# Kernel optimization log

Measured on AMD Instinct MI355X. Metric: run time of the kernel, lower is better.

Reference implementation:

```python
import jax, jax.numpy as jnp
import numpy as np

N = 100000
IN_DIM = 128
HID = 32
HEADS = 2
DEG = 16
NEG_SLOPE = 0.2


def setup_inputs() -> dict:
    rng = np.random.default_rng(0)
    E_rand = N * DEG
    src = np.concatenate([rng.integers(0, N, E_rand), np.arange(N)]).astype(np.int64)
    dst = np.concatenate([rng.integers(0, N, E_rand), np.arange(N)]).astype(np.int64)

    key = jax.random.key(0)
    ks = jax.random.split(key, 10)
    feat = jax.random.normal(ks[0], (N, IN_DIM), dtype=jnp.float32)
    # layer 1: in_dim -> HEADS * HID
    W1 = jax.random.normal(ks[1], (IN_DIM, HEADS * HID), dtype=jnp.float32) / np.sqrt(IN_DIM)
    al1 = jax.random.normal(ks[2], (HEADS, HID), dtype=jnp.float32) * 0.1
    ar1 = jax.random.normal(ks[3], (HEADS, HID), dtype=jnp.float32) * 0.1
    b1 = jnp.zeros((HEADS * HID,), dtype=jnp.float32)
    # layer 2: HEADS*HID -> 1 * HID
    W2 = jax.random.normal(ks[4], (HEADS * HID, HID), dtype=jnp.float32) / np.sqrt(HEADS * HID)
    al2 = jax.random.normal(ks[5], (1, HID), dtype=jnp.float32) * 0.1
    ar2 = jax.random.normal(ks[6], (1, HID), dtype=jnp.float32) * 0.1
    b2 = jnp.zeros((HID,), dtype=jnp.float32)
    return {"feat": feat, "W1": W1, "al1": al1, "ar1": ar1, "b1": b1,
            "W2": W2, "al2": al2, "ar2": ar2, "b2": b2,
            "src": jnp.asarray(src), "dst": jnp.asarray(dst)}


def gat_conv(feat, W, al, ar, b, src, dst, n_nodes, activation=True):
    # DGL GATConv: fc (no bias) -> per-head dot with attn vecs -> leaky_relu
    # edge score -> softmax over incoming edges of each dst -> scatter-add -> +bias -> relu
    H, D = al.shape
    h = (feat @ W).reshape(-1, H, D)                       # [N,H,D]
    el = jnp.einsum('nhd,hd->nh', h, al)                   # [N,H]
    er = jnp.einsum('nhd,hd->nh', h, ar)                   # [N,H]
    e = jax.nn.leaky_relu(el[src] + er[dst], NEG_SLOPE)    # [E,H]
    m = jax.ops.segment_max(e, dst, num_segments=n_nodes)  # [N,H]
    e = jnp.exp(e - jax.lax.stop_gradient(m)[dst])
    s = jax.ops.segment_sum(e, dst, num_segments=n_nodes)  # [N,H]
    a = e / s[dst]                                         # [E,H]
    msg = h[src] * a[:, :, None]                           # [E,H,D]
    out = jax.ops.segment_sum(msg, dst, num_segments=n_nodes)  # [N,H,D]
    out = out + b.reshape(1, H, D)
    return jax.nn.relu(out) if activation else out


def reference(feat, W1, al1, ar1, b1, W2, al2, ar2, b2, src, dst):
    h = gat_conv(feat, W1, al1, ar1, b1, src, dst, N)      # [N,HEADS,HID]
    h = h.reshape(h.shape[0], -1)                          # [N,HEADS*HID]
    h = gat_conv(h, W2, al2, ar2, b2, src, dst, N)         # [N,1,HID]
    return h.squeeze(1)                                    # [N,HID]
```

## Files before the change

### kernel.cpp

```cpp
#include <hip/hip_runtime.h>
#include <hip/hip_fp16.h>
#include <math.h>


constexpr int CAP  = 64;
constexpr int MAXB = 512;
constexpr int TILE = 2048;
constexpr int BCAP = 5120;

typedef _Float16 f16x8 __attribute__((ext_vector_type(8)));
typedef float    f32x4 __attribute__((ext_vector_type(4)));

__global__ __launch_bounds__(256)
void k_prew(const float* __restrict__ W1, const float* __restrict__ al1, const float* __restrict__ ar1,
            const float* __restrict__ W2, const float* __restrict__ al2, const float* __restrict__ ar2,
            _Float16* __restrict__ vh1, _Float16* __restrict__ B2h, int* __restrict__ gcur)
{
    const int t = threadIdx.x;
    for (int i = t; i < 128 * 16; i += 256) {
        const int k = i >> 4, c = i & 15;
        float s = 0.f;
        if (c < 4) {
            const int h = c & 1;
            const float* a = (c >> 1) ? ar1 : al1;
            #pragma unroll
            for (int d = 0; d < 32; d++) s += W1[k * 64 + h * 32 + d] * a[h * 32 + d];
        }
        vh1[i] = (_Float16)s;
    }
    for (int i = t; i < 64 * 64; i += 256) {
        const int k = i >> 6, c = i & 63;
        float s = 0.f;
        if (c < 32) s = W2[k * 32 + c];
        else if (c < 34) {
            const float* a = (c == 32) ? al2 : ar2;
            #pragma unroll
            for (int d = 0; d < 32; d++) s += W2[k * 32 + d] * a[d];
        }
        B2h[i] = (_Float16)s;
    }
    for (int b = t; b < MAXB; b += 256) gcur[b] = 0;
}

__global__ __launch_bounds__(256)
void k_front(const int* __restrict__ src, const int* __restrict__ dst,
             int* __restrict__ gcur, unsigned* __restrict__ binbuf, int E, int Gbin,
             const float* __restrict__ x, const float* __restrict__ W,
             const _Float16* __restrict__ vh1,
             __half* __restrict__ h1, float* __restrict__ el, float* __restrict__ er,
             int nnodes)
{
    __shared__ alignas(16) char smem[32 * 1024];
    const int tid = threadIdx.x;

    if ((int)blockIdx.x < Gbin) {
        int* cnt  = (int*)smem;
        int* base = cnt + MAXB;
        for (int b = tid; b < MAXB; b += 256) cnt[b] = 0;
        __syncthreads();
        const int e0 = blockIdx.x * TILE;
        int lo[8]; unsigned rec[8]; int bn[8];
        #pragma unroll
        for (int u = 0; u < 8; u++) {
            const int e = e0 + u * 256 + tid;
            if (e < E) {
                const int d = dst[e];
                bn[u]  = d >> 8;
                rec[u] = ((unsigned)src[e] << 8) | (unsigned)(d & 255);
                lo[u]  = atomicAdd(&cnt[bn[u]], 1);
            } else bn[u] = -1;
        }
        __syncthreads();
        for (int b = tid; b < MAXB; b += 256) {
            const int c = cnt[b];
            base[b] = c ? atomicAdd(&gcur[b], c) : 0;
        }
        __syncthreads();
        #pragma unroll
        for (int u = 0; u < 8; u++) if (bn[u] >= 0) {
            const int p = base[bn[u]] + lo[u];
            if ((unsigned)p < (unsigned)BCAP)
                binbuf[(long)bn[u] * BCAP + p] = rec[u];
        }
        return;
    }

    _Float16* xs = (_Float16*)smem;
    _Float16* Wh = xs + 64 * 128;
    const int node0 = ((int)blockIdx.x - Gbin) * 64;

    for (int c = tid; c < 1024; c += 256) {
        const int row = c >> 4, k8 = c & 15;
        const int n = node0 + row;
        float4 v0 = make_float4(0, 0, 0, 0), v1 = v0;
        if (n < nnodes) {
            v0 = ((const float4*)x)[(long)n * 32 + k8 * 2];
            v1 = ((const float4*)x)[(long)n * 32 + k8 * 2 + 1];
        }
        f16x8 h;
        h[0] = v0.x; h[1] = v0.y; h[2] = v0.z; h[3] = v0.w;
        h[4] = v1.x; h[5] = v1.y; h[6] = v1.z; h[7] = v1.w;
        const int off = (row * 256 + k8 * 16) ^ ((row & 7) << 4);
        *(f16x8*)((char*)xs + off) = h;
    }
    for (int c = tid; c < 1024; c += 256) {
        const int k = c >> 3, j8 = (c & 7) * 8;
        float4 v0 = ((const float4*)W)[(k * 64 + j8) >> 2];
        float4 v1 = ((const float4*)W)[((k * 64 + j8) >> 2) + 1];
        f16x8 h;
        h[0] = v0.x; h[1] = v0.y; h[2] = v0.z; h[3] = v0.w;
        h[4] = v1.x; h[5] = v1.y; h[6] = v1.z; h[7] = v1.w;
        *(f16x8*)(Wh + k * 64 + j8) = h;
    }
    __syncthreads();

    const int wv = tid >> 6, l = tid & 63;
    const int col = wv * 16 + (l & 15);
    const int g = l >> 4;
    f16x8 bfr[4], vfr[4];
    #pragma unroll
    for (int t = 0; t < 4; t++)
        #pragma unroll
        for (int e = 0; e < 8; e++)
            bfr[t][e] = Wh[(t * 32 + g * 8 + e) * 64 + col];
    if (wv == 0) {
        #pragma unroll
        for (int t = 0; t < 4; t++)
            #pragma unroll
            for (int e = 0; e < 8; e++)
                vfr[t][e] = vh1[(t * 32 + g * 8 + e) * 16 + (l & 15)];
    }

    #pragma unroll
    for (int nt = 0; nt < 4; nt++) {
        f32x4 acc = {0.f, 0.f, 0.f, 0.f}, accv = {0.f, 0.f, 0.f, 0.f};
        const int row = nt * 16 + (l & 15);
        #pragma unroll
        for (int t = 0; t < 4; t++) {
            const int off = (row * 256 + (t * 32 + g * 8) * 2) ^ ((row & 7) << 4);
            f16x8 af = *(const f16x8*)((const char*)xs + off);
            acc = __builtin_amdgcn_mfma_f32_16x16x32_f16(af, bfr[t], acc, 0, 0, 0);
            if (wv == 0)
                accv = __builtin_amdgcn_mfma_f32_16x16x32_f16(af, vfr[t], accv, 0, 0, 0);
        }
        #pragma unroll
        for (int r = 0; r < 4; r++) {
            const int n = node0 + nt * 16 + g * 4 + r;
            if (n < nnodes) {
                h1[(long)n * 64 + col] = __float2half((float)acc[r]);
                if (wv == 0) {
                    const int c4 = l & 15;
                    if (c4 < 2)      el[n * 2 + c4]       = (float)accv[r];
                    else if (c4 < 4) er[n * 2 + (c4 - 2)] = (float)accv[r];
                }
            }
        }
    }
}

__global__ __launch_bounds__(256)
void k_scatter(const unsigned* __restrict__ binbuf, const int* __restrict__ gcur,
               int* __restrict__ deg, int* __restrict__ bucket, int nnodes)
{
    extern __shared__ int lds[];
    int* ldeg  = lds;
    int* lbuck = lds + 256;
    const int t = threadIdx.x, b = blockIdx.x;
    const int nb0 = b << 8;
    ldeg[t] = 0;
    __syncthreads();
    const int cnt = min(max(gcur[b], 0), BCAP);
    const unsigned* recs = binbuf + (long)b * BCAP;
    for (int i = t; i < cnt; i += 256) {
        const unsigned r = recs[i];
        const int nl  = (int)(r & 255u);
        const int pos = atomicAdd(&ldeg[nl], 1);
        if (pos < CAP) lbuck[nl * CAP + pos] = (int)(r >> 8);
    }
    __syncthreads();
    const int nv = min(256, nnodes - nb0);
    if (t < nv) deg[nb0 + t] = ldeg[t];
    const int tot4 = nv * (CAP / 4);
    int4* gb = (int4*)(bucket + (long)nb0 * CAP);
    const int4* lb = (const int4*)lbuck;
    for (int i = t; i < tot4; i += 256) gb[i] = lb[i];
}

__global__ __launch_bounds__(256)
void k_agg1(const __half* __restrict__ hbuf, const float* __restrict__ el,
            const float* __restrict__ er, const int* __restrict__ deg,
            const int* __restrict__ bucket, const float* __restrict__ b1,
            __half* __restrict__ o1, int nnodes)
{
    constexpr int OUT = 64;
    const int w = threadIdx.x >> 6, lane = threadIdx.x & 63;
    const int n = blockIdx.x * 4 + w;
    __shared__ int    sbuf[4][CAP];
    __shared__ float2 wbuf[4][CAP];
    if (n >= nnodes) return;

    const int dn = min(deg[n], CAP);
    const int sv = (lane < dn) ? bucket[(long)n * CAP + lane] : 0;
    sbuf[w][lane] = sv;

    const float2 ernv = ((const float2*)er)[n];
    const float2 elv  = ((const float2*)el)[sv];
    float e0 = elv.x + ernv.x; e0 = (e0 > 0.f) ? e0 : 0.2f * e0;
    float e1 = elv.y + ernv.y; e1 = (e1 > 0.f) ? e1 : 0.2f * e1;
    const float w0 = (lane < dn) ? __expf(e0) : 0.f;
    const float w1 = (lane < dn) ? __expf(e1) : 0.f;
    wbuf[w][lane] = make_float2(w0, w1);
    float s0 = w0, s1 = w1;
    #pragma unroll
    for (int off = 32; off; off >>= 1) {
        s0 += __shfl_xor(s0, off, 64);
        s1 += __shfl_xor(s1, off, 64);
    }
    const float inv0 = (s0 > 0.f) ? 1.f / s0 : 0.f;
    const float inv1 = (s1 > 0.f) ? 1.f / s1 : 0.f;

    const int q = lane >> 3, c8 = lane & 7, hh = c8 >> 2;
    const float invC = hh ? inv1 : inv0;
    float acc[8] = {0.f,0.f,0.f,0.f,0.f,0.f,0.f,0.f};
    for (int i = 0; i < dn; i += 16) {
        const int   sA = sbuf[w][i + q],                     sB = sbuf[w][i + 8 + q];
        const float wA = ((const float*)&wbuf[w][i + q])[hh];
        const float wB = ((const float*)&wbuf[w][i + 8 + q])[hh];
        union { float4 f4; __half2 h2v[4]; } uA, uB;
        uA.f4 = *(const float4*)(hbuf + (long)sA * OUT + c8 * 8);
        uB.f4 = *(const float4*)(hbuf + (long)sB * OUT + c8 * 8);
        #pragma unroll
        for (int j = 0; j < 4; j++) {
            const float2 xa = __half22float2(uA.h2v[j]);
            const float2 xb = __half22float2(uB.h2v[j]);
            acc[2*j]   = fmaf(xa.x, wA, acc[2*j]);
            acc[2*j+1] = fmaf(xa.y, wA, acc[2*j+1]);
            acc[2*j]   = fmaf(xb.x, wB, acc[2*j]);
            acc[2*j+1] = fmaf(xb.y, wB, acc[2*j+1]);
        }
    }
    #pragma unroll
    for (int j = 0; j < 8; j++) {
        acc[j] += __shfl_xor(acc[j], 8, 64);
        acc[j] += __shfl_xor(acc[j], 16, 64);
        acc[j] += __shfl_xor(acc[j], 32, 64);
    }
    if (q == 0) {
        f16x8 ov;
        #pragma unroll
        for (int j = 0; j < 8; j++)
            ov[j] = (_Float16)fmaxf(acc[j] * invC + b1[c8 * 8 + j], 0.f);
        *(f16x8*)((char*)o1 + (long)n * 128 + c8 * 16) = ov;
    }
}

__global__ __launch_bounds__(256)
void k_gemm2(const __half* __restrict__ o1, const _Float16* __restrict__ B2h,
             __half* __restrict__ h2, float* __restrict__ el2, float* __restrict__ er2,
             int nnodes)
{
    __shared__ _Float16 xs[64 * 64];
    const int tid = threadIdx.x;
    const int node0 = blockIdx.x * 64;

    for (int c = tid; c < 512; c += 256) {
        const int row = c >> 3, k8 = c & 7;
        const int n = node0 + row;
        f16x8 h = {0,0,0,0,0,0,0,0};
        if (n < nnodes) h = *(const f16x8*)((const char*)o1 + (long)n * 128 + k8 * 16);
        const int off = (row * 128 + k8 * 16) ^ ((row & 7) << 4);
        *(f16x8*)((char*)xs + off) = h;
    }
    __syncthreads();

    const int wv = tid >> 6, l = tid & 63;
    if (wv == 3) return;
    const int col = wv * 16 + (l & 15);
    const int g = l >> 4;
    f16x8 bfr[2];
    #pragma unroll
    for (int t = 0; t < 2; t++)
        #pragma unroll
        for (int e = 0; e < 8; e++)
            bfr[t][e] = B2h[(t * 32 + g * 8 + e) * 64 + col];

    #pragma unroll
    for (int nt = 0; nt < 4; nt++) {
        f32x4 acc = {0.f, 0.f, 0.f, 0.f};
        const int row = nt * 16 + (l & 15);
        #pragma unroll
        for (int t = 0; t < 2; t++) {
            const int off = (row * 128 + (t * 32 + g * 8) * 2) ^ ((row & 7) << 4);
            f16x8 af = *(const f16x8*)((const char*)xs + off);
            acc = __builtin_amdgcn_mfma_f32_16x16x32_f16(af, bfr[t], acc, 0, 0, 0);
        }
        #pragma unroll
        for (int r = 0; r < 4; r++) {
            const int n = node0 + nt * 16 + g * 4 + r;
            if (n < nnodes) {
                if (wv < 2) h2[(long)n * 32 + col] = __float2half((float)acc[r]);
                else {
                    const int c4 = l & 15;
                    if (c4 == 0)      el2[n] = (float)acc[r];
                    else if (c4 == 1) er2[n] = (float)acc[r];
                }
            }
        }
    }
}

__global__ __launch_bounds__(256)
void k_agg2(const __half* __restrict__ h2, const float* __restrict__ el2,
            const float* __restrict__ er2, const int* __restrict__ deg,
            const int* __restrict__ bucket, const float* __restrict__ b2,
            float* __restrict__ out, int nnodes)
{
    const int w = threadIdx.x >> 6, lane = threadIdx.x & 63;
    const int n = blockIdx.x * 4 + w;
    __shared__ int   sbuf[4][CAP];
    __shared__ float wbuf[4][CAP];
    if (n >= nnodes) return;

    const int dn = min(deg[n], CAP);
    const int sv = (lane < dn) ? bucket[(long)n * CAP + lane] : 0;
    sbuf[w][lane] = sv;

    const float ern = er2[n];
    float e = el2[sv] + ern; e = (e > 0.f) ? e : 0.2f * e;
    const float wt = (lane < dn) ? __expf(e) : 0.f;
    wbuf[w][lane] = wt;
    float s = wt;
    #pragma unroll
    for (int off = 32; off; off >>= 1) s += __shfl_xor(s, off, 64);
    const float inv = (s > 0.f) ? 1.f / s : 0.f;

    const int q = lane >> 2, c8 = lane & 3;
    float acc[8] = {0.f,0.f,0.f,0.f,0.f,0.f,0.f,0.f};
    for (int i = 0; i < dn; i += 16) {
        const int   sA = sbuf[w][i + q];
        const float wA = wbuf[w][i + q];
        union { float4 f4; __half2 h2v[4]; } uA;
        uA.f4 = *(const float4*)(h2 + (long)sA * 32 + c8 * 8);
        #pragma unroll
        for (int j = 0; j < 4; j++) {
            const float2 xa = __half22float2(uA.h2v[j]);
            acc[2*j]   = fmaf(xa.x, wA, acc[2*j]);
            acc[2*j+1] = fmaf(xa.y, wA, acc[2*j+1]);
        }
    }
    #pragma unroll
    for (int j = 0; j < 8; j++) {
        acc[j] += __shfl_xor(acc[j], 4, 64);
        acc[j] += __shfl_xor(acc[j], 8, 64);
        acc[j] += __shfl_xor(acc[j], 16, 64);
        acc[j] += __shfl_xor(acc[j], 32, 64);
    }
    if (q == 0) {
        float r[8];
        #pragma unroll
        for (int j = 0; j < 8; j++)
            r[j] = fmaxf(acc[j] * inv + b2[c8 * 8 + j], 0.f);
        float4* po = (float4*)(out + (long)n * 32 + c8 * 8);
        po[0] = make_float4(r[0], r[1], r[2], r[3]);
        po[1] = make_float4(r[4], r[5], r[6], r[7]);
    }
}

extern "C" void kernel_launch(void* const* d_in, const int* in_sizes, int n_in,
                              void* d_out, int out_size, void* d_ws, size_t ws_size,
                              hipStream_t stream)
{
    const float* feat = (const float*)d_in[0];
    const float* W1   = (const float*)d_in[1];
    const float* al1  = (const float*)d_in[2];
    const float* ar1  = (const float*)d_in[3];
    const float* b1   = (const float*)d_in[4];
    const float* W2   = (const float*)d_in[5];
    const float* al2  = (const float*)d_in[6];
    const float* ar2  = (const float*)d_in[7];
    const float* b2   = (const float*)d_in[8];
    const int*   src  = (const int*)d_in[9];
    const int*   dst  = (const int*)d_in[10];

    const int N  = in_sizes[0] / 128;
    const int E  = in_sizes[9];
    const int NB = (N + 255) >> 8;

    char* ws = (char*)d_ws;
    size_t off = 0;
    auto alloc = [&](size_t bytes) -> void* {
        void* p = ws + off;
        off += (bytes + 255) & ~size_t(255);
        return p;
    };
    const size_t szA = ((size_t)NB * BCAP * 4 > (size_t)N * 64 * 2)
                     ? (size_t)NB * BCAP * 4 : (size_t)N * 64 * 2;
    char*     A      = (char*)    alloc(szA);
    unsigned* binbuf = (unsigned*)A;
    __half*   o1     = (__half*)  A;
    char*     B      = (char*)    alloc((size_t)N * 64 * 2);
    __half*   h1     = (__half*)  B;
    __half*   h2     = (__half*)  B;
    int*      gcur   = (int*)     alloc((size_t)MAXB * 4);
    int*      deg    = (int*)     alloc((size_t)N * 4);
    int*      bucket = (int*)     alloc((size_t)N * CAP * 4);
    float*    el1    = (float*)   alloc((size_t)N * 2 * 4);
    float*    er1    = (float*)   alloc((size_t)N * 2 * 4);
    float*    el2    = (float*)   alloc((size_t)N * 4);
    float*    er2    = (float*)   alloc((size_t)N * 4);
    _Float16* vh1    = (_Float16*)alloc(128 * 16 * 2);
    _Float16* B2h    = (_Float16*)alloc(64 * 64 * 2);

    const int Gbin  = (E + TILE - 1) / TILE;
    const int Ggemm = (N + 63) / 64;

    k_prew<<<1, 256, 0, stream>>>(W1, al1, ar1, W2, al2, ar2, vh1, B2h, gcur);
    k_front<<<Gbin + Ggemm, 256, 0, stream>>>(src, dst, gcur, binbuf, E, Gbin,
                                              feat, W1, vh1, h1, el1, er1, N);
    k_scatter<<<NB, 256, (256 + 256 * CAP) * 4, stream>>>(binbuf, gcur, deg, bucket, N);
    k_agg1<<<(N + 3) / 4, 256, 0, stream>>>(h1, el1, er1, deg, bucket, b1, o1, N);
    k_gemm2<<<(N + 63) / 64, 256, 0, stream>>>(o1, B2h, h2, el2, er2, N);
    k_agg2<<<(N + 3) / 4, 256, 0, stream>>>(h2, el2, er2, deg, bucket, b2,
                                            (float*)d_out, N);
}
```

Measured before the change: 281.7 us.

## Fuse back-end stages into one cooperative kernel and compact adjacency via prefix scan

Removes the weight-precompute kernel: el/er for layer 1 are now computed from an LDS-staged h tile after the GEMM, and the layer-2 weight prep runs inside the back kernel. The fixed-capacity bucket array is replaced by a compacted CSR-like adjacency built with a block prefix scan and a global atomic offset. The agg1, gemm2 and agg2 kernels are merged into one persistent cooperative kernel with grid-wide syncs between phases. This cuts launch overhead and the padded bucket traffic, at the cost of grid syncs, a grid capped by occupancy, and serial per-thread adjacency writes in the scatter kernel.

Result: slower. 599.4 us (+112.7%).

```diff
diff --git a/kernel.cpp b/kernel.cpp
--- a/kernel.cpp
+++ b/kernel.cpp
@@ -1,52 +1,25 @@
 #include <hip/hip_runtime.h>
 #include <hip/hip_fp16.h>
+#include <hip/hip_cooperative_groups.h>
 #include <math.h>
+
+namespace cg = cooperative_groups;
 
 
 constexpr int CAP  = 64;
 constexpr int MAXB = 512;
 constexpr int TILE = 2048;
 constexpr int BCAP = 5120;
+constexpr int HTS  = 72;
 
 typedef _Float16 f16x8 __attribute__((ext_vector_type(8)));
 typedef float    f32x4 __attribute__((ext_vector_type(4)));
-
-__global__ __launch_bounds__(256)
-void k_prew(const float* __restrict__ W1, const float* __restrict__ al1, const float* __restrict__ ar1,
-            const float* __restrict__ W2, const float* __restrict__ al2, const float* __restrict__ ar2,
-            _Float16* __restrict__ vh1, _Float16* __restrict__ B2h, int* __restrict__ gcur)
-{
-    const int t = threadIdx.x;
-    for (int i = t; i < 128 * 16; i += 256) {
-        const int k = i >> 4, c = i & 15;
-        float s = 0.f;
-        if (c < 4) {
-            const int h = c & 1;
-            const float* a = (c >> 1) ? ar1 : al1;
-            #pragma unroll
-            for (int d = 0; d < 32; d++) s += W1[k * 64 + h * 32 + d] * a[h * 32 + d];
-        }
-        vh1[i] = (_Float16)s;
-    }
-    for (int i = t; i < 64 * 64; i += 256) {
-        const int k = i >> 6, c = i & 63;
-        float s = 0.f;
-        if (c < 32) s = W2[k * 32 + c];
-        else if (c < 34) {
-            const float* a = (c == 32) ? al2 : ar2;
-            #pragma unroll
-            for (int d = 0; d < 32; d++) s += W2[k * 32 + d] * a[d];
-        }
-        B2h[i] = (_Float16)s;
-    }
-    for (int b = t; b < MAXB; b += 256) gcur[b] = 0;
-}
 
 __global__ __launch_bounds__(256)
 void k_front(const int* __restrict__ src, const int* __restrict__ dst,
              int* __restrict__ gcur, unsigned* __restrict__ binbuf, int E, int Gbin,
              const float* __restrict__ x, const float* __restrict__ W,
-             const _Float16* __restrict__ vh1,
+             const float* __restrict__ al1, const float* __restrict__ ar1,
              __half* __restrict__ h1, float* __restrict__ el, float* __restrict__ er,
              int nnodes)
 {
@@ -117,54 +90,64 @@
     const int wv = tid >> 6, l = tid & 63;
     const int col = wv * 16 + (l & 15);
     const int g = l >> 4;
-    f16x8 bfr[4], vfr[4];
+    f16x8 bfr[4];
     #pragma unroll
     for (int t = 0; t < 4; t++)
         #pragma unroll
         for (int e = 0; e < 8; e++)
             bfr[t][e] = Wh[(t * 32 + g * 8 + e) * 64 + col];
-    if (wv == 0) {
-        #pragma unroll
-        for (int t = 0; t < 4; t++)
-            #pragma unroll
-            for (int e = 0; e < 8; e++)
-                vfr[t][e] = vh1[(t * 32 + g * 8 + e) * 16 + (l & 15)];
-    }
-
+
+    f32x4 accs[4];
     #pragma unroll
     for (int nt = 0; nt < 4; nt++) {
-        f32x4 acc = {0.f, 0.f, 0.f, 0.f}, accv = {0.f, 0.f, 0.f, 0.f};
+        f32x4 acc = {0.f, 0.f, 0.f, 0.f};
         const int row = nt * 16 + (l & 15);
         #pragma unroll
         for (int t = 0; t < 4; t++) {
             const int off = (row * 256 + (t * 32 + g * 8) * 2) ^ ((row & 7) << 4);
             f16x8 af = *(const f16x8*)((const char*)xs + off);
             acc = __builtin_amdgcn_mfma_f32_16x16x32_f16(af, bfr[t], acc, 0, 0, 0);
-            if (wv == 0)
-                accv = __builtin_amdgcn_mfma_f32_16x16x32_f16(af, vfr[t], accv, 0, 0, 0);
-        }
+        }
+        accs[nt] = acc;
+    }
+    __syncthreads();
+
+    _Float16* htile = xs;
+    #pragma unroll
+    for (int nt = 0; nt < 4; nt++) {
         #pragma unroll
         for (int r = 0; r < 4; r++) {
-            const int n = node0 + nt * 16 + g * 4 + r;
-            if (n < nnodes) {
-                h1[(long)n * 64 + col] = __float2half((float)acc[r]);
-                if (wv == 0) {
-                    const int c4 = l & 15;
-                    if (c4 < 2)      el[n * 2 + c4]       = (float)accv[r];
-                    else if (c4 < 4) er[n * 2 + (c4 - 2)] = (float)accv[r];
-                }
-            }
-        }
+            const int nl = nt * 16 + g * 4 + r;
+            const float v = (float)accs[nt][r];
+            htile[nl * HTS + col] = (_Float16)v;
+            const int n = node0 + nl;
+            if (n < nnodes) h1[(long)n * 64 + col] = __float2half(v);
+        }
+    }
+    __syncthreads();
+
+    const int nodeL = tid >> 2, c4 = tid & 3, hh = c4 & 1;
+    const float* av = ((c4 >> 1) ? ar1 : al1) + hh * 32;
+    const _Float16* hrow = htile + nodeL * HTS + hh * 32;
+    float sacc = 0.f;
+    #pragma unroll
+    for (int d = 0; d < 32; d++) sacc = fmaf((float)hrow[d], av[d], sacc);
+    const int n = node0 + nodeL;
+    if (n < nnodes) {
+        if (c4 < 2) el[(long)n * 2 + hh] = sacc;
+        else        er[(long)n * 2 + hh] = sacc;
     }
 }
 
 __global__ __launch_bounds__(256)
-void k_scatter(const unsigned* __restrict__ binbuf, const int* __restrict__ gcur,
-               int* __restrict__ deg, int* __restrict__ bucket, int nnodes)
+void k_scatter(const unsigned* __restrict__ binbuf, int* __restrict__ gcur,
+               int2* __restrict__ ndesc, int* __restrict__ eadj, int nnodes)
 {
     extern __shared__ int lds[];
     int* ldeg  = lds;
-    int* lbuck = lds + 256;
+    int* lscan = lds + 256;
+    int* lbuck = lds + 512;
+    __shared__ int sbase;
     const int t = threadIdx.x, b = blockIdx.x;
     const int nb0 = b << 8;
     ldeg[t] = 0;
@@ -175,194 +158,227 @@
         const unsigned r = recs[i];
         const int nl  = (int)(r & 255u);
         const int pos = atomicAdd(&ldeg[nl], 1);
-        if (pos < CAP) lbuck[nl * CAP + pos] = (int)(r >> 8);
-    }
-    __syncthreads();
-    const int nv = min(256, nnodes - nb0);
-    if (t < nv) deg[nb0 + t] = ldeg[t];
-    const int tot4 = nv * (CAP / 4);
-    int4* gb = (int4*)(bucket + (long)nb0 * CAP);
-    const int4* lb = (const int4*)lbuck;
-    for (int i = t; i < tot4; i += 256) gb[i] = lb[i];
+        if (pos < CAP) lbuck[pos * 256 + nl] = (int)(r >> 8);
+    }
+    __syncthreads();
+    const int dn = min(ldeg[t], CAP);
+    lscan[t] = dn;
+    __syncthreads();
+    for (int o = 1; o < 256; o <<= 1) {
+        const int v = lscan[t];
+        const int u = (t >= o) ? lscan[t - o] : 0;
+        __syncthreads();
+        lscan[t] = v + u;
+        __syncthreads();
+    }
+    if (t == 0) sbase = atomicAdd(&gcur[MAXB], lscan[255]);
+    __syncthreads();
+    const int start = sbase + lscan[t] - dn;
+    const int n = nb0 + t;
+    if (n < nnodes) ndesc[n] = make_int2(start, dn);
+    for (int i = 0; i < dn; i++) eadj[start + i] = lbuck[i * 256 + t];
 }
 
-__global__ __launch_bounds__(256)
-void k_agg1(const __half* __restrict__ hbuf, const float* __restrict__ el,
-            const float* __restrict__ er, const int* __restrict__ deg,
-            const int* __restrict__ bucket, const float* __restrict__ b1,
-            __half* __restrict__ o1, int nnodes)
-{
-    constexpr int OUT = 64;
-    const int w = threadIdx.x >> 6, lane = threadIdx.x & 63;
-    const int n = blockIdx.x * 4 + w;
-    __shared__ int    sbuf[4][CAP];
-    __shared__ float2 wbuf[4][CAP];
-    if (n >= nnodes) return;
-
-    const int dn = min(deg[n], CAP);
-    const int sv = (lane < dn) ? bucket[(long)n * CAP + lane] : 0;
-    sbuf[w][lane] = sv;
-
-    const float2 ernv = ((const float2*)er)[n];
-    const float2 elv  = ((const float2*)el)[sv];
-    float e0 = elv.x + ernv.x; e0 = (e0 > 0.f) ? e0 : 0.2f * e0;
-    float e1 = elv.y + ernv.y; e1 = (e1 > 0.f) ? e1 : 0.2f * e1;
-    const float w0 = (lane < dn) ? __expf(e0) : 0.f;
-    const float w1 = (lane < dn) ? __expf(e1) : 0.f;
-    wbuf[w][lane] = make_float2(w0, w1);
-    float s0 = w0, s1 = w1;
-    #pragma unroll
-    for (int off = 32; off; off >>= 1) {
-        s0 += __shfl_xor(s0, off, 64);
-        s1 += __shfl_xor(s1, off, 64);
-    }
-    const float inv0 = (s0 > 0.f) ? 1.f / s0 : 0.f;
-    const float inv1 = (s1 > 0.f) ? 1.f / s1 : 0.f;
-
-    const int q = lane >> 3, c8 = lane & 7, hh = c8 >> 2;
-    const float invC = hh ? inv1 : inv0;
-    float acc[8] = {0.f,0.f,0.f,0.f,0.f,0.f,0.f,0.f};
-    for (int i = 0; i < dn; i += 16) {
-        const int   sA = sbuf[w][i + q],                     sB = sbuf[w][i + 8 + q];
-        const float wA = ((const float*)&wbuf[w][i + q])[hh];
-        const float wB = ((const float*)&wbuf[w][i + 8 + q])[hh];
-        union { float4 f4; __half2 h2v[4]; } uA, uB;
-        uA.f4 = *(const float4*)(hbuf + (long)sA * OUT + c8 * 8);
-        uB.f4 = *(const float4*)(hbuf + (long)sB * OUT + c8 * 8);
-        #pragma unroll
-        for (int j = 0; j < 4; j++) {
-            const float2 xa = __half22float2(uA.h2v[j]);
-            const float2 xb = __half22float2(uB.h2v[j]);
-            acc[2*j]   = fmaf(xa.x, wA, acc[2*j]);
-            acc[2*j+1] = fmaf(xa.y, wA, acc[2*j+1]);
-            acc[2*j]   = fmaf(xb.x, wB, acc[2*j]);
-            acc[2*j+1] = fmaf(xb.y, wB, acc[2*j+1]);
-        }
-    }
-    #pragma unroll
-    for (int j = 0; j < 8; j++) {
-        acc[j] += __shfl_xor(acc[j], 8, 64);
-        acc[j] += __shfl_xor(acc[j], 16, 64);
-        acc[j] += __shfl_xor(acc[j], 32, 64);
-    }
-    if (q == 0) {
-        f16x8 ov;
-        #pragma unroll
-        for (int j = 0; j < 8; j++)
-            ov[j] = (_Float16)fmaxf(acc[j] * invC + b1[c8 * 8 + j], 0.f);
-        *(f16x8*)((char*)o1 + (long)n * 128 + c8 * 16) = ov;
-    }
-}
-
-__global__ __launch_bounds__(256)
-void k_gemm2(const __half* __restrict__ o1, const _Float16* __restrict__ B2h,
-             __half* __restrict__ h2, float* __restrict__ el2, float* __restrict__ er2,
-             int nnodes)
-{
-    __shared__ _Float16 xs[64 * 64];
-    const int tid = threadIdx.x;
-    const int node0 = blockIdx.x * 64;
-
-    for (int c = tid; c < 512; c += 256) {
-        const int row = c >> 3, k8 = c & 7;
-        const int n = node0 + row;
-        f16x8 h = {0,0,0,0,0,0,0,0};
-        if (n < nnodes) h = *(const f16x8*)((const char*)o1 + (long)n * 128 + k8 * 16);
-        const int off = (row * 128 + k8 * 16) ^ ((row & 7) << 4);
-        *(f16x8*)((char*)xs + off) = h;
-    }
-    __syncthreads();
-
-    const int wv = tid >> 6, l = tid & 63;
-    if (wv == 3) return;
-    const int col = wv * 16 + (l & 15);
-    const int g = l >> 4;
-    f16x8 bfr[2];
-    #pragma unroll
-    for (int t = 0; t < 2; t++)
-        #pragma unroll
-        for (int e = 0; e < 8; e++)
-            bfr[t][e] = B2h[(t * 32 + g * 8 + e) * 64 + col];
-
-    #pragma unroll
-    for (int nt = 0; nt < 4; nt++) {
-        f32x4 acc = {0.f, 0.f, 0.f, 0.f};
-        const int row = nt * 16 + (l & 15);
-        #pragma unroll
-        for (int t = 0; t < 2; t++) {
-            const int off = (row * 128 + (t * 32 + g * 8) * 2) ^ ((row & 7) << 4);
-            f16x8 af = *(const f16x8*)((const char*)xs + off);
-            acc = __builtin_amdgcn_mfma_f32_16x16x32_f16(af, bfr[t], acc, 0, 0, 0);
-        }
-        #pragma unroll
-        for (int r = 0; r < 4; r++) {
-            const int n = node0 + nt * 16 + g * 4 + r;
-            if (n < nnodes) {
-                if (wv < 2) h2[(long)n * 32 + col] = __float2half((float)acc[r]);
-                else {
-                    const int c4 = l & 15;
-                    if (c4 == 0)      el2[n] = (float)acc[r];
-                    else if (c4 == 1) er2[n] = (float)acc[r];
-                }
-            }
-        }
-    }
-}
-
-__global__ __launch_bounds__(256)
-void k_agg2(const __half* __restrict__ h2, const float* __restrict__ el2,
-            const float* __restrict__ er2, const int* __restrict__ deg,
-            const int* __restrict__ bucket, const float* __restrict__ b2,
+__global__ __launch_bounds__(256, 8)
+void k_back(const __half* __restrict__ h1, const float* __restrict__ el1,
+            const float* __restrict__ er1, const int2* __restrict__ ndesc,
+            const int* __restrict__ eadj, const float* __restrict__ b1,
+            const float* __restrict__ W2, const float* __restrict__ al2,
+            const float* __restrict__ ar2, const float* __restrict__ b2,
+            __half* __restrict__ o1, __half* __restrict__ h2,
+            float* __restrict__ el2, float* __restrict__ er2,
             float* __restrict__ out, int nnodes)
 {
+    __shared__ alignas(16) char smem[16 * 1024];
+    cg::grid_group gg = cg::this_grid();
     const int w = threadIdx.x >> 6, lane = threadIdx.x & 63;
-    const int n = blockIdx.x * 4 + w;
-    __shared__ int   sbuf[4][CAP];
-    __shared__ float wbuf[4][CAP];
-    if (n >= nnodes) return;
-
-    const int dn = min(deg[n], CAP);
-    const int sv = (lane < dn) ? bucket[(long)n * CAP + lane] : 0;
-    sbuf[w][lane] = sv;
-
-    const float ern = er2[n];
-    float e = el2[sv] + ern; e = (e > 0.f) ? e : 0.2f * e;
-    const float wt = (lane < dn) ? __expf(e) : 0.f;
-    wbuf[w][lane] = wt;
-    float s = wt;
-    #pragma unroll
-    for (int off = 32; off; off >>= 1) s += __shfl_xor(s, off, 64);
-    const float inv = (s > 0.f) ? 1.f / s : 0.f;
-
-    const int q = lane >> 2, c8 = lane & 3;
-    float acc[8] = {0.f,0.f,0.f,0.f,0.f,0.f,0.f,0.f};
-    for (int i = 0; i < dn; i += 16) {
-        const int   sA = sbuf[w][i + q];
-        const float wA = wbuf[w][i + q];
-        union { float4 f4; __half2 h2v[4]; } uA;
-        uA.f4 = *(const float4*)(h2 + (long)sA * 32 + c8 * 8);
-        #pragma unroll
-        for (int j = 0; j < 4; j++) {
-            const float2 xa = __half22float2(uA.h2v[j]);
-            acc[2*j]   = fmaf(xa.x, wA, acc[2*j]);
-            acc[2*j+1] = fmaf(xa.y, wA, acc[2*j+1]);
-        }
-    }
-    #pragma unroll
-    for (int j = 0; j < 8; j++) {
-        acc[j] += __shfl_xor(acc[j], 4, 64);
-        acc[j] += __shfl_xor(acc[j], 8, 64);
-        acc[j] += __shfl_xor(acc[j], 16, 64);
-        acc[j] += __shfl_xor(acc[j], 32, 64);
-    }
-    if (q == 0) {
-        float r[8];
-        #pragma unroll
-        for (int j = 0; j < 8; j++)
-            r[j] = fmaxf(acc[j] * inv + b2[c8 * 8 + j], 0.f);
-        float4* po = (float4*)(out + (long)n * 32 + c8 * 8);
-        po[0] = make_float4(r[0], r[1], r[2], r[3]);
-        po[1] = make_float4(r[4], r[5], r[6], r[7]);
+
+    {
+        int*    sb = (int*)smem;
+        float2* wb = (float2*)(smem + 1024);
+        const int NB4 = (nnodes + 3) >> 2;
+        for (int vb = blockIdx.x; vb < NB4; vb += gridDim.x) {
+            const int n = vb * 4 + w;
+            if (n >= nnodes) continue;
+            const int2 nd = ndesc[n];
+            const int dn = nd.y;
+            const int sv = (lane < dn) ? eadj[nd.x + lane] : 0;
+            sb[w * 64 + lane] = sv;
+
+            const float2 ernv = ((const float2*)er1)[n];
+            const float2 elv  = ((const float2*)el1)[sv];
+            float e0 = elv.x + ernv.x; e0 = (e0 > 0.f) ? e0 : 0.2f * e0;
+            float e1 = elv.y + ernv.y; e1 = (e1 > 0.f) ? e1 : 0.2f * e1;
+            const float w0 = (lane < dn) ? __expf(e0) : 0.f;
+            const float w1 = (lane < dn) ? __expf(e1) : 0.f;
+            wb[w * 64 + lane] = make_float2(w0, w1);
+            float s0 = w0, s1 = w1;
+            #pragma unroll
+            for (int off = 32; off; off >>= 1) {
+                s0 += __shfl_xor(s0, off, 64);
+                s1 += __shfl_xor(s1, off, 64);
+            }
+            const float inv0 = (s0 > 0.f) ? 1.f / s0 : 0.f;
+            const float inv1 = (s1 > 0.f) ? 1.f / s1 : 0.f;
+
+            const int q = lane >> 3, c8 = lane & 7, hh = c8 >> 2;
+            const float invC = hh ? inv1 : inv0;
+            float acc[8] = {0.f,0.f,0.f,0.f,0.f,0.f,0.f,0.f};
+            for (int i = 0; i < dn; i += 16) {
+                const int   sA = sb[w * 64 + i + q],  sB = sb[w * 64 + i + 8 + q];
+                const float wA = ((const float*)&wb[w * 64 + i + q])[hh];
+                const float wB = ((const float*)&wb[w * 64 + i + 8 + q])[hh];
+                union { float4 f4; __half2 h2v[4]; } uA, uB;
+                uA.f4 = *(const float4*)(h1 + (long)sA * 64 + c8 * 8);
+                uB.f4 = *(const float4*)(h1 + (long)sB * 64 + c8 * 8);
+                #pragma unroll
+                for (int j = 0; j < 4; j++) {
+                    const float2 xa = __half22float2(uA.h2v[j]);
+                    const float2 xb = __half22float2(uB.h2v[j]);
+                    acc[2*j]   = fmaf(xa.x, wA, acc[2*j]);
+                    acc[2*j+1] = fmaf(xa.y, wA, acc[2*j+1]);
+                    acc[2*j]   = fmaf(xb.x, wB, acc[2*j]);
+                    acc[2*j+1] = fmaf(xb.y, wB, acc[2*j+1]);
+                }
+            }
+            #pragma unroll
+            for (int j = 0; j < 8; j++) {
+                acc[j] += __shfl_xor(acc[j], 8, 64);
+                acc[j] += __shfl_xor(acc[j], 16, 64);
+                acc[j] += __shfl_xor(acc[j], 32, 64);
+            }
+            if (q == 0) {
+                f16x8 ov;
+                #pragma unroll
+                for (int j = 0; j < 8; j++)
+                    ov[j] = (_Float16)fmaxf(acc[j] * invC + b1[c8 * 8 + j], 0.f);
+                *(f16x8*)((char*)o1 + (long)n * 128 + c8 * 16) = ov;
+            }
+        }
+    }
+    gg.sync();
+
+    {
+        _Float16* B2s = (_Float16*)smem;
+        _Float16* xs  = (_Float16*)(smem + 8192);
+        for (int i = threadIdx.x; i < 64 * 64; i += 256) {
+            const int k = i >> 6, c = i & 63;
+            float s = 0.f;
+            if (c < 32) s = W2[k * 32 + c];
+            else if (c < 34) {
+                const float* a = (c == 32) ? al2 : ar2;
+                #pragma unroll
+                for (int d = 0; d < 32; d++) s += W2[k * 32 + d] * a[d];
+            }
+            B2s[i] = (_Float16)s;
+        }
+        __syncthreads();
+
+        const int wv = threadIdx.x >> 6, l = threadIdx.x & 63;
+        const int col = wv * 16 + (l & 15);
+        const int g2 = l >> 4;
+        f16x8 bfr[2];
+        if (wv < 3) {
+            #pragma unroll
+            for (int t = 0; t < 2; t++)
+                #pragma unroll
+                for (int e = 0; e < 8; e++)
+                    bfr[t][e] = B2s[(t * 32 + g2 * 8 + e) * 64 + col];
+        }
+        const int NB64 = (nnodes + 63) >> 6;
+        for (int vb = blockIdx.x; vb < NB64; vb += gridDim.x) {
+            const int node0 = vb * 64;
+            for (int cc = threadIdx.x; cc < 512; cc += 256) {
+                const int row = cc >> 3, k8 = cc & 7;
+                const int n = node0 + row;
+                f16x8 hv = {0,0,0,0,0,0,0,0};
+                if (n < nnodes) hv = *(const f16x8*)((const char*)o1 + (long)n * 128 + k8 * 16);
+                const int off = (row * 128 + k8 * 16) ^ ((row & 7) << 4);
+                *(f16x8*)((char*)xs + off) = hv;
+            }
+            __syncthreads();
+            if (wv < 3) {
+                #pragma unroll
+                for (int nt = 0; nt < 4; nt++) {
+                    f32x4 acc = {0.f, 0.f, 0.f, 0.f};
+                    const int row = nt * 16 + (l & 15);
+                    #pragma unroll
+                    for (int t = 0; t < 2; t++) {
+                        const int off = (row * 128 + (t * 32 + g2 * 8) * 2) ^ ((row & 7) << 4);
+                        f16x8 af = *(const f16x8*)((const char*)xs + off);
+                        acc = __builtin_amdgcn_mfma_f32_16x16x32_f16(af, bfr[t], acc, 0, 0, 0);
+                    }
+                    #pragma unroll
+                    for (int r = 0; r < 4; r++) {
+                        const int n = node0 + nt * 16 + g2 * 4 + r;
+                        if (n < nnodes) {
+                            if (wv < 2) h2[(long)n * 32 + col] = __float2half((float)acc[r]);
+                            else {
+                                const int cc4 = l & 15;
+                                if (cc4 == 0)      el2[n] = (float)acc[r];
+                                else if (cc4 == 1) er2[n] = (float)acc[r];
+                            }
+                        }
+                    }
+                }
+            }
+            __syncthreads();
+        }
+    }
+    gg.sync();
+
+    {
+        int*   sb = (int*)smem;
+        float* wb = (float*)(smem + 1024);
+        const int NB4 = (nnodes + 3) >> 2;
+        for (int vb = blockIdx.x; vb < NB4; vb += gridDim.x) {
+            const int n = vb * 4 + w;
+            if (n >= nnodes) continue;
+            const int2 nd = ndesc[n];
+            const int dn = nd.y;
+            const int sv = (lane < dn) ? eadj[nd.x + lane] : 0;
+            sb[w * 64 + lane] = sv;
+
+            const float ern = er2[n];
+            float e = el2[sv] + ern; e = (e > 0.f) ? e : 0.2f * e;
+            const float wt = (lane < dn) ? __expf(e) : 0.f;
+            wb[w * 64 + lane] = wt;
+            float s = wt;
+            #pragma unroll
+            for (int off = 32; off; off >>= 1) s += __shfl_xor(s, off, 64);
+            const float inv = (s > 0.f) ? 1.f / s : 0.f;
+
+            const int q = lane >> 2, c8 = lane & 3;
+            float acc[8] = {0.f,0.f,0.f,0.f,0.f,0.f,0.f,0.f};
+            for (int i = 0; i < dn; i += 16) {
+                const int   sA = sb[w * 64 + i + q];
+                const float wA = wb[w * 64 + i + q];
+                union { float4 f4; __half2 h2v[4]; } uA;
+                uA.f4 = *(const float4*)(h2 + (long)sA * 32 + c8 * 8);
+                #pragma unroll
+                for (int j = 0; j < 4; j++) {
+                    const float2 xa = __half22float2(uA.h2v[j]);
+                    acc[2*j]   = fmaf(xa.x, wA, acc[2*j]);
+                    acc[2*j+1] = fmaf(xa.y, wA, acc[2*j+1]);
+                }
+            }
+            #pragma unroll
+            for (int j = 0; j < 8; j++) {
+                acc[j] += __shfl_xor(acc[j], 4, 64);
+                acc[j] += __shfl_xor(acc[j], 8, 64);
+                acc[j] += __shfl_xor(acc[j], 16, 64);
+                acc[j] += __shfl_xor(acc[j], 32, 64);
+            }
+            if (q == 0) {
+                float r[8];
+                #pragma unroll
+                for (int j = 0; j < 8; j++)
+                    r[j] = fmaxf(acc[j] * inv + b2[c8 * 8 + j], 0.f);
+                float4* po = (float4*)(out + (long)n * 32 + c8 * 8);
+                po[0] = make_float4(r[0], r[1], r[2], r[3]);
+                po[1] = make_float4(r[4], r[5], r[6], r[7]);
+            }
+        }
     }
 }
 
@@ -398,28 +414,39 @@
     char*     A      = (char*)    alloc(szA);
     unsigned* binbuf = (unsigned*)A;
     __half*   o1     = (__half*)  A;
-    char*     B      = (char*)    alloc((size_t)N * 64 * 2);
-    __half*   h1     = (__half*)  B;
-    __half*   h2     = (__half*)  B;
-    int*      gcur   = (int*)     alloc((size_t)MAXB * 4);
-    int*      deg    = (int*)     alloc((size_t)N * 4);
-    int*      bucket = (int*)     alloc((size_t)N * CAP * 4);
+    char*     Br     = (char*)    alloc((size_t)N * 64 * 2);
+    __half*   h1     = (__half*)  Br;
+    __half*   h2     = (__half*)  Br;
+    int*      gcur   = (int*)     alloc((size_t)(MAXB + 1) * 4);
+    int2*     ndesc  = (int2*)    alloc((size_t)N * 8);
+    int*      eadj   = (int*)     alloc((size_t)E * 4);
     float*    el1    = (float*)   alloc((size_t)N * 2 * 4);
     float*    er1    = (float*)   alloc((size_t)N * 2 * 4);
     float*    el2    = (float*)   alloc((size_t)N * 4);
     float*    er2    = (float*)   alloc((size_t)N * 4);
-    _Float16* vh1    = (_Float16*)alloc(128 * 16 * 2);
-    _Float16* B2h    = (_Float16*)alloc(64 * 64 * 2);
+
+    hipMemsetAsync(gcur, 0, (size_t)(MAXB + 1) * 4, stream);
 
     const int Gbin  = (E + TILE - 1) / TILE;
     const int Ggemm = (N + 63) / 64;
 
-    k_prew<<<1, 256, 0, stream>>>(W1, al1, ar1, W2, al2, ar2, vh1, B2h, gcur);
     k_front<<<Gbin + Ggemm, 256, 0, stream>>>(src, dst, gcur, binbuf, E, Gbin,
-                                              feat, W1, vh1, h1, el1, er1, N);
-    k_scatter<<<NB, 256, (256 + 256 * CAP) * 4, stream>>>(binbuf, gcur, deg, bucket, N);
-    k_agg1<<<(N + 3) / 4, 256, 0, stream>>>(h1, el1, er1, deg, bucket, b1, o1, N);
-    k_gemm2<<<(N + 63) / 64, 256, 0, stream>>>(o1, B2h, h2, el2, er2, N);
-    k_agg2<<<(N + 3) / 4, 256, 0, stream>>>(h2, el2, er2, deg, bucket, b2,
-                                            (float*)d_out, N);
+                                              feat, W1, al1, ar1, h1, el1, er1, N);
+    k_scatter<<<NB, 256, (512 + 256 * CAP) * 4, stream>>>(binbuf, gcur, ndesc, eadj, N);
+
+    int nbm = 0;
+    hipOccupancyMaxActiveBlocksPerMultiprocessor(&nbm, (const void*)k_back, 256, 0);
+    if (nbm < 1) nbm = 1;
+    long grid = (long)nbm * 256;
+    const long NB4 = ((long)N + 3) / 4;
+    if (grid > NB4) grid = NB4;
+    if (grid > 2048) grid = 2048;
+
+    void* h1v = (void*)h1;  void* o1v = (void*)o1;  void* h2v = (void*)h2;
+    int   Nv  = N;
+    void* args[] = {&h1v, (void*)&el1, (void*)&er1, (void*)&ndesc, (void*)&eadj,
+                    (void*)&b1, (void*)&W2, (void*)&al2, (void*)&ar2, (void*)&b2,
+                    &o1v, &h2v, (void*)&el2, (void*)&er2, (void*)&d_out, &Nv};
+    hipLaunchCooperativeKernel((const void*)k_back, dim3((unsigned)grid), dim3(256),
+                               args, 0, stream);
 }
```
